# Optimization experiments

Hardware: AMD Instinct MI355X
Metric: run time of the kernel (lower is better)

The kernel has to match this reference:

```python
import jax, jax.numpy as jnp
import numpy as np

N_NODES, N_EDGES, N_GRAPHS, H = 20000, 160000, 256, 128
EPS = 1e-5


def setup_inputs() -> dict:
    key = jax.random.key(0)
    it = iter(jax.random.split(key, 64))

    def nk():
        return next(it)

    def lin(fan_in, wshape, bshape):
        s = 1.0 / np.sqrt(fan_in)
        W = jax.random.uniform(nk(), wshape, jnp.float32, -s, s)
        b = jax.random.uniform(nk(), bshape, jnp.float32, -s, s)
        return W, b

    def bn_params(shape):
        g = 1.0 + 0.1 * jax.random.normal(nk(), shape, jnp.float32)
        b = 0.1 * jax.random.normal(nk(), shape, jnp.float32)
        m = 0.1 * jax.random.normal(nk(), shape, jnp.float32)
        v = jax.random.uniform(nk(), shape, jnp.float32, 0.5, 1.5)
        return g, b, m, v

    inp = {}
    inp["x"] = jax.random.normal(nk(), (N_NODES, 10), jnp.float32)
    inp["edge_attr"] = jax.random.normal(nk(), (N_EDGES, 3), jnp.float32)
    inp["edge_index"] = jax.random.randint(nk(), (2, N_EDGES), 0, N_NODES)
    inp["batch"] = jnp.sort(jax.random.randint(nk(), (N_NODES,), 0, N_GRAPHS))
    inp["W_node"], inp["b_node"] = lin(10, (10, H), (H,))
    inp["W_edge"], inp["b_edge"] = lin(3, (3, H), (H,))
    # 10 stacked CGConv layers: lin_f / lin_s each map [2H + H] -> H
    inp["Wf"], inp["bf"] = lin(3 * H, (10, 3 * H, H), (10, H))
    inp["Ws"], inp["bs"] = lin(3 * H, (10, 3 * H, H), (10, H))
    inp["bn_g"], inp["bn_b"], inp["bn_m"], inp["bn_v"] = bn_params((10, H))
    inp["W1"], inp["b1"] = lin(3 * H, (3 * H, 2 * H), (2 * H,))
    inp["bn1_g"], inp["bn1_b"], inp["bn1_m"], inp["bn1_v"] = bn_params((2 * H,))
    inp["W2"], inp["b2"] = lin(2 * H, (2 * H, H), (H,))
    inp["bn2_g"], inp["bn2_b"], inp["bn2_m"], inp["bn2_v"] = bn_params((H,))
    inp["W3"], inp["b3"] = lin(H, (H, H // 2), (H // 2,))
    inp["Wv"], inp["bv"] = lin(H // 2, (H // 2, 1), (1,))
    inp["W_en"], inp["b_en"] = lin(H // 2, (H // 2, 1), (1,))
    inp["Wd"], inp["bd"] = lin(H // 2, (H // 2, 1), (1,))
    inp["Wh"], inp["bh"] = lin(H // 2, (H // 2, 1), (1,))
    return inp


def reference(x, edge_attr, edge_index, batch, W_node, b_node, W_edge, b_edge,
              Wf, bf, Ws, bs, bn_g, bn_b, bn_m, bn_v,
              W1, b1, bn1_g, bn1_b, bn1_m, bn1_v,
              W2, b2, bn2_g, bn2_b, bn2_m, bn2_v,
              W3, b3, Wv, bv, W_en, b_en, Wd, bd, Wh, bh):
    h = jax.nn.relu(x @ W_node + b_node)             # [N, H]
    e = jax.nn.relu(edge_attr @ W_edge + b_edge)     # [E, H]
    src, dst = edge_index[0], edge_index[1]          # PyG: messages src -> dst
    n = h.shape[0]
    for i in range(10):  # fixed layer count, structurally distinct weights
        h_in = h
        z = jnp.concatenate([h[dst], h[src], e], axis=1)          # [E, 3H] = [x_i, x_j, e_ij]
        msg = jax.nn.sigmoid(z @ Wf[i] + bf[i]) * jax.nn.softplus(z @ Ws[i] + bs[i])
        h = h_in + jax.ops.segment_sum(msg, dst, num_segments=n)  # CGConv residual + add-aggr
        h = (h - bn_m[i]) * (bn_g[i] / jnp.sqrt(bn_v[i] + EPS)) + bn_b[i]  # BN (eval)
        h = jax.nn.relu(h)  # dropout is identity in eval
        if i % 2 == 1:
            h = h + h_in
    # global mean / max / add pooling over graphs
    s = jax.ops.segment_sum(h, batch, num_segments=N_GRAPHS)                     # [G, H]
    cnt = jax.ops.segment_sum(jnp.ones((n, 1), h.dtype), batch, num_segments=N_GRAPHS)
    mean = s / jnp.maximum(cnt, 1.0)
    mx = jax.ops.segment_max(h, batch, num_segments=N_GRAPHS)
    g = jnp.concatenate([mean, mx, s], axis=1)                                   # [G, 3H]
    g = jax.nn.relu((g @ W1 + b1 - bn1_m) * (bn1_g / jnp.sqrt(bn1_v + EPS)) + bn1_b)
    g = jax.nn.relu((g @ W2 + b2 - bn2_m) * (bn2_g / jnp.sqrt(bn2_v + EPS)) + bn2_b)
    g = jax.nn.relu(g @ W3 + b3)
    return (g @ Wv + bv, g @ W_en + b_en, g @ Wd + bd, g @ Wh + bh)
```

## Files before the change

kernel.cpp:

```cpp
#include <hip/hip_runtime.h>
#include <hip/hip_bf16.h>
#include <math.h>

#define NN 20000
#define NE 160000
#define NG 256
#define EPSV 1e-5f
#define NQB 2500

typedef short bf16x8 __attribute__((ext_vector_type(8)));
typedef unsigned short u16x8 __attribute__((ext_vector_type(8)));
typedef float f32x4 __attribute__((ext_vector_type(4)));

__device__ __forceinline__ unsigned short f2bf(float f){
  unsigned int u = __float_as_uint(f);
  unsigned int r = (u + 0x7fffu + ((u>>16)&1u)) >> 16;
  return (unsigned short)r;
}
__device__ __forceinline__ float bf2f(unsigned short h){
  return __uint_as_float(((unsigned int)h) << 16);
}
__device__ __forceinline__ float fastmsg(float f, float sv){
  float sg = __builtin_amdgcn_rcpf(1.0f + __expf(-f));
  float sp = fmaxf(sv, 0.0f) + __logf(1.0f + __expf(-fabsf(sv)));
  return sg * sp;
}

__global__ __launch_bounds__(256) void k_hist(const int* __restrict__ ei, int* __restrict__ deg){
  int e = blockIdx.x*256 + threadIdx.x;
  if (e < NE) atomicAdd(&deg[ei[NE+e]], 1);
}
__global__ __launch_bounds__(1024) void k_scan(const int* __restrict__ deg,
                                               int* __restrict__ start, int* __restrict__ cur){
  __shared__ int part[1024];
  int t = threadIdx.x;
  int base = t*20;
  int s = 0;
  for (int j=0;j<20;j++){ int i = base+j; if (i<NN) s += deg[i]; }
  part[t] = s; __syncthreads();
  for (int off=1; off<1024; off<<=1){
    int v = (t >= off) ? part[t-off] : 0;
    __syncthreads();
    part[t] += v;
    __syncthreads();
  }
  int run = (t>0) ? part[t-1] : 0;
  for (int j=0;j<20;j++){
    int i = base+j;
    if (i<NN){ start[i] = run; cur[i] = run; run += deg[i]; }
  }
}
__global__ __launch_bounds__(256) void k_scatter(
    const int* __restrict__ ei, const float* __restrict__ eattr,
    int* __restrict__ cur, int* __restrict__ ei_s, int* __restrict__ ei_d,
    float* __restrict__ ea_s){
  int e = blockIdx.x*256 + threadIdx.x;
  if (e >= NE) return;
  int d = ei[NE+e];
  int p = atomicAdd(&cur[d], 1);
  ei_s[p] = ei[e]; ei_d[p] = d;
  ea_s[p*3+0] = eattr[e*3+0];
  ea_s[p*3+1] = eattr[e*3+1];
  ea_s[p*3+2] = eattr[e*3+2];
}

__global__ __launch_bounds__(256) void k_pack_w(
    const float* __restrict__ Wf, const float* __restrict__ Ws,
    unsigned short* __restrict__ Wpk_hi, unsigned short* __restrict__ Wpk_md,
    unsigned short* __restrict__ Wpk_lo)
{
  int idx = blockIdx.x*256 + threadIdx.x;
  if (idx >= 122880) return;
  int l = idx & 63, ks = (idx>>6)&3, nt = (idx>>8)&7;
  int m = idx >> 11;
  int blk = m % 3, gL = m / 3;
  int g = gL & 1, L = gL >> 1;
  const float* src = (g ? Ws : Wf) + (size_t)L*384*128;
  size_t off = (size_t)m*16384 + (nt*4+ks)*512 + l*8;
  int col = nt*16 + (l&15), k0 = ks*32 + (l>>4)*8;
  #pragma unroll
  for (int j=0;j<8;j++){
    float w = src[(size_t)(blk*128 + k0 + j)*128 + col];
    unsigned short hi = f2bf(w);
    float r1 = w - bf2f(hi);
    unsigned short md = f2bf(r1);
    float r2 = r1 - bf2f(md);
    Wpk_hi[off+j] = hi;
    Wpk_md[off+j] = md;
    Wpk_lo[off+j] = f2bf(r2);
  }
}

__global__ __launch_bounds__(256) void k_embed_node(
    const float* __restrict__ x, const float* __restrict__ W, const float* __restrict__ b,
    float* __restrict__ h, float* __restrict__ hacc)
{
  int i = blockIdx.x*256 + threadIdx.x;
  if (i >= NN*128) return;
  int n = i >> 7, c = i & 127;
  float acc = b[c];
  const float* xr = x + n*10;
  #pragma unroll
  for (int k=0;k<10;k++) acc = fmaf(xr[k], W[k*128+c], acc);
  acc = fmaxf(acc, 0.0f);
  h[i] = acc; hacc[i] = acc;
}

__global__ __launch_bounds__(512,1) void k_nodeproj_mfma(
    const float* __restrict__ h,
    const unsigned short* __restrict__ Wpk_hi, const unsigned short* __restrict__ Wpk_md,
    const unsigned short* __restrict__ Wpk_lo,
    const float* __restrict__ bfv, const float* __restrict__ bsv,
    float* __restrict__ Pd, float* __restrict__ Ps)
{
  __shared__ unsigned short wsm[49152];
  int bid = blockIdx.x;
  int m_idx = bid / 157, nblk = bid - m_idx*157;
  int mm = (m_idx==0)?0:(m_idx==1)?1:(m_idx==2)?3:4;
  int t = threadIdx.x;
  {
    const unsigned short* s0 = Wpk_hi + (size_t)mm*16384;
    const unsigned short* s1 = Wpk_md + (size_t)mm*16384;
    const unsigned short* s2 = Wpk_lo + (size_t)mm*16384;
    #pragma unroll
    for (int ii=0; ii<4; ii++){
      int o = (t + ii*512)*8;
      *(u16x8*)(wsm + o)         = *(const u16x8*)(s0 + o);
      *(u16x8*)(wsm + 16384 + o) = *(const u16x8*)(s1 + o);
      *(u16x8*)(wsm + 32768 + o) = *(const u16x8*)(s2 + o);
    }
  }
  __syncthreads();
  int l = t & 63, w = t >> 6;
  int nb = nblk*128 + w*16;
  if (nb + 16 > NN) return;
  const float* hb = h + (size_t)(nb + (l&15))*128 + (l>>4)*8;
  bf16x8 ah[4], am[4], al[4];
  #pragma unroll
  for (int ks=0;ks<4;ks++){
    #pragma unroll
    for (int j=0;j<8;j++){
      float v = hb[ks*32 + j];
      unsigned short x0 = f2bf(v);
      float r1 = v - bf2f(x0);
      unsigned short x1 = f2bf(r1);
      float r2 = r1 - bf2f(x1);
      ah[ks][j] = (short)x0; am[ks][j] = (short)x1; al[ks][j] = (short)f2bf(r2);
    }
  }
  float* OUT = (m_idx & 1) ? Ps : Pd;
  int sel = (m_idx >= 2) ? 1 : 0;
  const float* bias = (m_idx==0) ? bfv : (m_idx==2) ? bsv : nullptr;
  int col0 = l & 15, rg = (l>>4)*4;
  #pragma unroll
  for (int nt=0; nt<8; nt++){
    f32x4 c = {0.f,0.f,0.f,0.f};
    #pragma unroll
    for (int ks=0;ks<4;ks++){
      int fo = (nt*4+ks)*512 + l*8;
      bf16x8 bh = *(const bf16x8*)(wsm + fo);
      bf16x8 bm = *(const bf16x8*)(wsm + 16384 + fo);
      bf16x8 bl = *(const bf16x8*)(wsm + 32768 + fo);
      c = __builtin_amdgcn_mfma_f32_16x16x32_bf16(al[ks], bh, c, 0,0,0);
      c = __builtin_amdgcn_mfma_f32_16x16x32_bf16(am[ks], bm, c, 0,0,0);
      c = __builtin_amdgcn_mfma_f32_16x16x32_bf16(ah[ks], bl, c, 0,0,0);
      c = __builtin_amdgcn_mfma_f32_16x16x32_bf16(am[ks], bh, c, 0,0,0);
      c = __builtin_amdgcn_mfma_f32_16x16x32_bf16(ah[ks], bm, c, 0,0,0);
      c = __builtin_amdgcn_mfma_f32_16x16x32_bf16(ah[ks], bh, c, 0,0,0);
    }
    float bb = bias ? bias[nt*16+col0] : 0.0f;
    #pragma unroll
    for (int r=0;r<4;r++)
      OUT[(size_t)(nb+rg+r)*256 + (nt*16+col0)*2 + sel] = c[r] + bb;
  }
}

__global__ __launch_bounds__(256,4) void k_edge_mfma(
    const float* __restrict__ ea_s, const float* __restrict__ W_edge,
    const float* __restrict__ b_edge,
    const unsigned short* __restrict__ Wpk_hi,
    const unsigned short* __restrict__ Wpk_md,
    const int* __restrict__ ei_s, const int* __restrict__ ei_d,
    const float* __restrict__ Pd, const float* __restrict__ Ps,
    float* __restrict__ hacc)
{
  __shared__ float wlds[512];
  __shared__ unsigned short bfr[16384];
  int bid = blockIdx.x;
  int q = bid / NQB, eg = bid - q*NQB;
  int t = threadIdx.x;
  for (int i=t;i<512;i+=256) wlds[i] = (i<384)? W_edge[i] : b_edge[i-384];
  #pragma unroll
  for (int ii=0; ii<8; ii++){
    int idx = t + ii*256;
    int f = idx >> 6;
    int off = (idx & 63) * 8;
    int g = f >> 4, term = (f>>3)&1, ntl = (f>>2)&1, ks = f&3;
    const unsigned short* src = (term ? Wpk_md : Wpk_hi)
        + (size_t)(g?5:2)*16384 + (size_t)((((q*2+ntl)*4+ks)*512) + off);
    *(u16x8*)(bfr + f*512 + off) = *(const u16x8*)src;
  }
  __syncthreads();
  int l = t & 63, w = t >> 6;
  int e0 = eg*64;
  int row_edge = e0 + w*16 + (l&15);
  float a0 = ea_s[row_edge*3+0], a1 = ea_s[row_edge*3+1], a2 = ea_s[row_edge*3+2];
  int cbase = (l>>4)*8;
  bf16x8 ah[4], al[4];
  #pragma unroll
  for (int ks=0;ks<4;ks++){
    #pragma unroll
    for (int j=0;j<8;j++){
      int c = cbase + ks*32 + j;
      float v = fmaf(a0, wlds[c], fmaf(a1, wlds[128+c], fmaf(a2, wlds[256+c], wlds[384+c])));
      v = fmaxf(v, 0.0f);
      unsigned short hi = f2bf(v);
      ah[ks][j] = (short)hi;
      al[ks][j] = (short)f2bf(v - bf2f(hi));
    }
  }
  f32x4 accf[2], accs[2];
  #pragma unroll
  for (int ntl=0; ntl<2; ntl++){
    f32x4 cf = {0.f,0.f,0.f,0.f}, cs = {0.f,0.f,0.f,0.f};
    #pragma unroll
    for (int ks=0; ks<4; ks++){
      bf16x8 bh = *(const bf16x8*)(bfr + ((0<<4)|(0<<3)|(ntl<<2)|ks)*512 + l*8);
      bf16x8 bm = *(const bf16x8*)(bfr + ((0<<4)|(1<<3)|(ntl<<2)|ks)*512 + l*8);
      cf = __builtin_amdgcn_mfma_f32_16x16x32_bf16(ah[ks], bh, cf, 0,0,0);
      cf = __builtin_amdgcn_mfma_f32_16x16x32_bf16(ah[ks], bm, cf, 0,0,0);
      cf = __builtin_amdgcn_mfma_f32_16x16x32_bf16(al[ks], bh, cf, 0,0,0);
      bf16x8 sh = *(const bf16x8*)(bfr + ((1<<4)|(0<<3)|(ntl<<2)|ks)*512 + l*8);
      bf16x8 sm = *(const bf16x8*)(bfr + ((1<<4)|(1<<3)|(ntl<<2)|ks)*512 + l*8);
      cs = __builtin_amdgcn_mfma_f32_16x16x32_bf16(ah[ks], sh, cs, 0,0,0);
      cs = __builtin_amdgcn_mfma_f32_16x16x32_bf16(ah[ks], sm, cs, 0,0,0);
      cs = __builtin_amdgcn_mfma_f32_16x16x32_bf16(al[ks], sh, cs, 0,0,0);
    }
    accf[ntl] = cf; accs[ntl] = cs;
  }
  int eb = e0 + w*16, col0 = l & 15, rg = (l>>4)*4;
  int cA = (q*2+0)*16 + col0;
  int cB = (q*2+1)*16 + col0;
  int prev_d = -1;
  float m0 = 0.f, m1 = 0.f;
  float2 pd0, pd1;
  #pragma unroll
  for (int r=0;r<4;r++){
    int p = eb + rg + r;
    int s = ei_s[p], d = ei_d[p];
    if (d != prev_d){
      if (prev_d >= 0){
        atomicAdd(hacc + (size_t)prev_d*128 + cA, m0);
        atomicAdd(hacc + (size_t)prev_d*128 + cB, m1);
      }
      prev_d = d;
      pd0 = *(const float2*)(Pd + (size_t)d*256 + cA*2);
      pd1 = *(const float2*)(Pd + (size_t)d*256 + cB*2);
      m0 = 0.f; m1 = 0.f;
    }
    float2 ps0 = *(const float2*)(Ps + (size_t)s*256 + cA*2);
    float2 ps1 = *(const float2*)(Ps + (size_t)s*256 + cB*2);
    m0 += fastmsg(accf[0][r] + pd0.x + ps0.x, accs[0][r] + pd0.y + ps0.y);
    m1 += fastmsg(accf[1][r] + pd1.x + ps1.x, accs[1][r] + pd1.y + ps1.y);
  }
  atomicAdd(hacc + (size_t)prev_d*128 + cA, m0);
  atomicAdd(hacc + (size_t)prev_d*128 + cB, m1);
}

__global__ __launch_bounds__(256) void k_bn(
    const float* __restrict__ hacc, const float* __restrict__ hin,
    const float* __restrict__ gam, const float* __restrict__ bet,
    const float* __restrict__ mu, const float* __restrict__ var,
    float* __restrict__ hout, float* __restrict__ haccout, int addres)
{
  int i = blockIdx.x*256 + threadIdx.x;
  if (i >= NN*128) return;
  int c = i & 127;
  float scale = gam[c]*rsqrtf(var[c]+EPSV);
  float tv = (hacc[i]-mu[c])*scale + bet[c];
  tv = fmaxf(tv, 0.0f);
  if (addres) tv += hin[i];
  hout[i] = tv; haccout[i] = tv;
}

__global__ __launch_bounds__(256) void k_pool(
    const float* __restrict__ h, const int* __restrict__ batch,
    float* __restrict__ psum, float* __restrict__ pmax, float* __restrict__ pcnt)
{
  int i = blockIdx.x*256 + threadIdx.x;
  if (i >= NN*128) return;
  int n = i >> 7, c = i & 127;
  int b = batch[n];
  float v = h[i];
  atomicAdd(&psum[b*128+c], v);
  atomicMax((unsigned int*)&pmax[b*128+c], __float_as_uint(v));
  if (c == 0) atomicAdd(&pcnt[b], 1.0f);
}

__global__ __launch_bounds__(256) void k_mlp1(
    const float* __restrict__ psum, const float* __restrict__ pmax, const float* __restrict__ pcnt,
    const float* __restrict__ W1, const float* __restrict__ b1,
    const float* __restrict__ g1g, const float* __restrict__ g1b,
    const float* __restrict__ g1m, const float* __restrict__ g1v,
    float* __restrict__ out)
{
  int i = blockIdx.x*256 + threadIdx.x;
  int g = i >> 8, c = i & 255;
  float inv = 1.0f / fmaxf(pcnt[g], 1.0f);
  float acc = b1[c];
  for (int k=0;k<128;k++) acc = fmaf(psum[g*128+k]*inv, W1[k*256+c], acc);
  for (int k=0;k<128;k++) acc = fmaf(pmax[g*128+k],     W1[(128+k)*256+c], acc);
  for (int k=0;k<128;k++) acc = fmaf(psum[g*128+k],     W1[(256+k)*256+c], acc);
  float scale = g1g[c]*rsqrtf(g1v[c]+EPSV);
  acc = (acc - g1m[c])*scale + g1b[c];
  out[i] = fmaxf(acc, 0.0f);
}

__global__ __launch_bounds__(256) void k_mlp2(
    const float* __restrict__ g1, const float* __restrict__ W2, const float* __restrict__ b2,
    const float* __restrict__ g2g, const float* __restrict__ g2b,
    const float* __restrict__ g2m, const float* __restrict__ g2v,
    float* __restrict__ out)
{
  int i = blockIdx.x*256 + threadIdx.x;
  int g = i >> 7, c = i & 127;
  float acc = b2[c];
  for (int k=0;k<256;k++) acc = fmaf(g1[g*256+k], W2[k*128+c], acc);
  float scale = g2g[c]*rsqrtf(g2v[c]+EPSV);
  acc = (acc - g2m[c])*scale + g2b[c];
  out[i] = fmaxf(acc, 0.0f);
}

__global__ __launch_bounds__(256) void k_mlp3(
    const float* __restrict__ g2, const float* __restrict__ W3, const float* __restrict__ b3,
    float* __restrict__ out)
{
  int i = blockIdx.x*256 + threadIdx.x;
  int g = i >> 6, c = i & 63;
  float acc = b3[c];
  for (int k=0;k<128;k++) acc = fmaf(g2[g*128+k], W3[k*64+c], acc);
  out[i] = fmaxf(acc, 0.0f);
}

__global__ __launch_bounds__(256) void k_heads(
    const float* __restrict__ g3,
    const float* __restrict__ Wv, const float* __restrict__ bv,
    const float* __restrict__ We, const float* __restrict__ be,
    const float* __restrict__ Wd, const float* __restrict__ bd,
    const float* __restrict__ Wh, const float* __restrict__ bh,
    float* __restrict__ out)
{
  int g = blockIdx.x*256 + threadIdx.x;
  if (g >= NG) return;
  float a0=bv[0], a1=be[0], a2=bd[0], a3=bh[0];
  for (int k=0;k<64;k++){
    float xv = g3[g*64+k];
    a0 = fmaf(xv, Wv[k], a0);
    a1 = fmaf(xv, We[k], a1);
    a2 = fmaf(xv, Wd[k], a2);
    a3 = fmaf(xv, Wh[k], a3);
  }
  out[g] = a0; out[NG+g] = a1; out[2*NG+g] = a2; out[3*NG+g] = a3;
}

extern "C" void kernel_launch(void* const* d_in, const int* in_sizes, int n_in,
                              void* d_out, int out_size, void* d_ws, size_t ws_size,
                              hipStream_t stream)
{
  const float* x         = (const float*)d_in[0];
  const float* edge_attr = (const float*)d_in[1];
  const int*   ei        = (const int*)d_in[2];
  const int*   batch     = (const int*)d_in[3];
  const float* W_node    = (const float*)d_in[4];
  const float* b_node    = (const float*)d_in[5];
  const float* W_edge    = (const float*)d_in[6];
  const float* b_edge    = (const float*)d_in[7];
  const float* Wf        = (const float*)d_in[8];
  const float* bf        = (const float*)d_in[9];
  const float* Ws        = (const float*)d_in[10];
  const float* bs        = (const float*)d_in[11];
  const float* bn_g      = (const float*)d_in[12];
  const float* bn_b      = (const float*)d_in[13];
  const float* bn_m      = (const float*)d_in[14];
  const float* bn_v      = (const float*)d_in[15];
  const float* W1        = (const float*)d_in[16];
  const float* b1        = (const float*)d_in[17];
  const float* bn1_g     = (const float*)d_in[18];
  const float* bn1_b     = (const float*)d_in[19];
  const float* bn1_m     = (const float*)d_in[20];
  const float* bn1_v     = (const float*)d_in[21];
  const float* W2        = (const float*)d_in[22];
  const float* b2        = (const float*)d_in[23];
  const float* bn2_g     = (const float*)d_in[24];
  const float* bn2_b     = (const float*)d_in[25];
  const float* bn2_m     = (const float*)d_in[26];
  const float* bn2_v     = (const float*)d_in[27];
  const float* W3        = (const float*)d_in[28];
  const float* b3        = (const float*)d_in[29];
  const float* Wv        = (const float*)d_in[30];
  const float* bv        = (const float*)d_in[31];
  const float* W_en      = (const float*)d_in[32];
  const float* b_en      = (const float*)d_in[33];
  const float* Wd        = (const float*)d_in[34];
  const float* bd        = (const float*)d_in[35];
  const float* Wh        = (const float*)d_in[36];
  const float* bh        = (const float*)d_in[37];

  float* wsf  = (float*)d_ws;
  float* h    = wsf;
  float* hacc = wsf + 2560000;
  float* Pd   = wsf + 5120000;
  float* Ps   = wsf + 10240000;
  unsigned short* Wpk_hi = (unsigned short*)(wsf + 15360000);
  unsigned short* Wpk_md = (unsigned short*)(wsf + 15851520);
  unsigned short* Wpk_lo = (unsigned short*)(wsf + 16343040);
  float* psum = wsf + 16834560;
  float* pmax = psum + 32768;
  float* pcnt = pmax + 32768;
  float* g1   = pcnt + 256;
  float* g2   = g1 + 65536;
  float* g3   = g2 + 32768;
  int*   deg  = (int*)(wsf + 16982272);
  int*   start= deg + 20000;
  int*   cur  = start + 20000;
  int*   ei_s = cur + 20000;
  int*   ei_d = ei_s + 160000;
  float* ea_s = (float*)(ei_d + 160000);

  hipMemsetAsync(deg, 0, 20000*sizeof(int), stream);
  k_hist<<<(NE+255)/256, 256, 0, stream>>>(ei, deg);
  k_scan<<<1, 1024, 0, stream>>>(deg, start, cur);
  k_scatter<<<(NE+255)/256, 256, 0, stream>>>(ei, edge_attr, cur, ei_s, ei_d, ea_s);

  k_pack_w<<<480, 256, 0, stream>>>(Wf, Ws, Wpk_hi, Wpk_md, Wpk_lo);
  k_embed_node<<<(NN*128+255)/256, 256, 0, stream>>>(x, W_node, b_node, h, hacc);
  hipMemsetAsync(psum, 0, (size_t)(32768+32768+256)*sizeof(float), stream);

  for (int i=0;i<10;i++){
    const unsigned short* WH = Wpk_hi + (size_t)i*6*16384;
    const unsigned short* WM = Wpk_md + (size_t)i*6*16384;
    const unsigned short* WL = Wpk_lo + (size_t)i*6*16384;
    k_nodeproj_mfma<<<628, 512, 0, stream>>>(h, WH, WM, WL,
        bf + i*128, bs + i*128, Pd, Ps);
    k_edge_mfma<<<4*NQB, 256, 0, stream>>>(ea_s, W_edge, b_edge,
        WH, WM, ei_s, ei_d, Pd, Ps, hacc);
    k_bn<<<(NN*128+255)/256, 256, 0, stream>>>(hacc, h,
        bn_g + i*128, bn_b + i*128, bn_m + i*128, bn_v + i*128, h, hacc, i&1);
  }

  k_pool<<<(NN*128+255)/256, 256, 0, stream>>>(h, batch, psum, pmax, pcnt);
  k_mlp1<<<(NG*256)/256, 256, 0, stream>>>(psum, pmax, pcnt, W1, b1, bn1_g, bn1_b, bn1_m, bn1_v, g1);
  k_mlp2<<<(NG*128)/256, 256, 0, stream>>>(g1, W2, b2, bn2_g, bn2_b, bn2_m, bn2_v, g2);
  k_mlp3<<<(NG*64)/256, 256, 0, stream>>>(g2, W3, b3, g3);
  k_heads<<<1, 256, 0, stream>>>(g3, Wv, bv, W_en, b_en, Wd, bd, Wh, bh, (float*)d_out);
}
```

Measured before the change: 1.424 ms.

## Cut nodeproj LDS to raise occupancy, pack edge indices, fuse final BN with pooling

The node projection kernel now keeps only the hi and mid weight planes in LDS and reads the lo plane straight from global memory. This shrinks shared memory so two blocks can run per CU, at the cost of extra global or cache traffic per MFMA step. The bf16 hi and mid splits now truncate instead of round, which saves instructions while keeping the three-term split exact enough. Source and destination indices are packed into one int2 array so each edge needs a single load, and the last layer's BN is fused with global pooling, removing one elementwise pass and one launch.

Result: faster. 1.302 ms (-8.6%).

```diff
diff --git a/kernel.cpp b/kernel.cpp
--- a/kernel.cpp
+++ b/kernel.cpp
@@ -52,13 +52,12 @@
 }
 __global__ __launch_bounds__(256) void k_scatter(
     const int* __restrict__ ei, const float* __restrict__ eattr,
-    int* __restrict__ cur, int* __restrict__ ei_s, int* __restrict__ ei_d,
-    float* __restrict__ ea_s){
+    int* __restrict__ cur, int2* __restrict__ esd, float* __restrict__ ea_s){
   int e = blockIdx.x*256 + threadIdx.x;
   if (e >= NE) return;
   int d = ei[NE+e];
   int p = atomicAdd(&cur[d], 1);
-  ei_s[p] = ei[e]; ei_d[p] = d;
+  esd[p] = make_int2(ei[e], d);
   ea_s[p*3+0] = eattr[e*3+0];
   ea_s[p*3+1] = eattr[e*3+1];
   ea_s[p*3+2] = eattr[e*3+2];
@@ -106,14 +105,14 @@
   h[i] = acc; hacc[i] = acc;
 }
 
-__global__ __launch_bounds__(512,1) void k_nodeproj_mfma(
+__global__ __launch_bounds__(512,2) void k_nodeproj_mfma(
     const float* __restrict__ h,
     const unsigned short* __restrict__ Wpk_hi, const unsigned short* __restrict__ Wpk_md,
     const unsigned short* __restrict__ Wpk_lo,
     const float* __restrict__ bfv, const float* __restrict__ bsv,
     float* __restrict__ Pd, float* __restrict__ Ps)
 {
-  __shared__ unsigned short wsm[49152];
+  __shared__ unsigned short wsm[32768];
   int bid = blockIdx.x;
   int m_idx = bid / 157, nblk = bid - m_idx*157;
   int mm = (m_idx==0)?0:(m_idx==1)?1:(m_idx==2)?3:4;
@@ -121,13 +120,11 @@
   {
     const unsigned short* s0 = Wpk_hi + (size_t)mm*16384;
     const unsigned short* s1 = Wpk_md + (size_t)mm*16384;
-    const unsigned short* s2 = Wpk_lo + (size_t)mm*16384;
     #pragma unroll
     for (int ii=0; ii<4; ii++){
       int o = (t + ii*512)*8;
       *(u16x8*)(wsm + o)         = *(const u16x8*)(s0 + o);
       *(u16x8*)(wsm + 16384 + o) = *(const u16x8*)(s1 + o);
-      *(u16x8*)(wsm + 32768 + o) = *(const u16x8*)(s2 + o);
     }
   }
   __syncthreads();
@@ -141,13 +138,14 @@
     #pragma unroll
     for (int j=0;j<8;j++){
       float v = hb[ks*32 + j];
-      unsigned short x0 = f2bf(v);
+      unsigned short x0 = (unsigned short)(__float_as_uint(v) >> 16);
       float r1 = v - bf2f(x0);
-      unsigned short x1 = f2bf(r1);
+      unsigned short x1 = (unsigned short)(__float_as_uint(r1) >> 16);
       float r2 = r1 - bf2f(x1);
       ah[ks][j] = (short)x0; am[ks][j] = (short)x1; al[ks][j] = (short)f2bf(r2);
     }
   }
+  const unsigned short* wl = Wpk_lo + (size_t)mm*16384 + l*8;
   float* OUT = (m_idx & 1) ? Ps : Pd;
   int sel = (m_idx >= 2) ? 1 : 0;
   const float* bias = (m_idx==0) ? bfv : (m_idx==2) ? bsv : nullptr;
@@ -160,7 +158,7 @@
       int fo = (nt*4+ks)*512 + l*8;
       bf16x8 bh = *(const bf16x8*)(wsm + fo);
       bf16x8 bm = *(const bf16x8*)(wsm + 16384 + fo);
-      bf16x8 bl = *(const bf16x8*)(wsm + 32768 + fo);
+      bf16x8 bl = *(const bf16x8*)(wl + (nt*4+ks)*512);
       c = __builtin_amdgcn_mfma_f32_16x16x32_bf16(al[ks], bh, c, 0,0,0);
       c = __builtin_amdgcn_mfma_f32_16x16x32_bf16(am[ks], bm, c, 0,0,0);
       c = __builtin_amdgcn_mfma_f32_16x16x32_bf16(ah[ks], bl, c, 0,0,0);
@@ -180,7 +178,7 @@
     const float* __restrict__ b_edge,
     const unsigned short* __restrict__ Wpk_hi,
     const unsigned short* __restrict__ Wpk_md,
-    const int* __restrict__ ei_s, const int* __restrict__ ei_d,
+    const int2* __restrict__ esd,
     const float* __restrict__ Pd, const float* __restrict__ Ps,
     float* __restrict__ hacc)
 {
@@ -214,7 +212,7 @@
       int c = cbase + ks*32 + j;
       float v = fmaf(a0, wlds[c], fmaf(a1, wlds[128+c], fmaf(a2, wlds[256+c], wlds[384+c])));
       v = fmaxf(v, 0.0f);
-      unsigned short hi = f2bf(v);
+      unsigned short hi = (unsigned short)(__float_as_uint(v) >> 16);
       ah[ks][j] = (short)hi;
       al[ks][j] = (short)f2bf(v - bf2f(hi));
     }
@@ -247,7 +245,8 @@
   #pragma unroll
   for (int r=0;r<4;r++){
     int p = eb + rg + r;
-    int s = ei_s[p], d = ei_d[p];
+    int2 sd = esd[p];
+    int s = sd.x, d = sd.y;
     if (d != prev_d){
       if (prev_d >= 0){
         atomicAdd(hacc + (size_t)prev_d*128 + cA, m0);
@@ -283,17 +282,24 @@
   hout[i] = tv; haccout[i] = tv;
 }
 
-__global__ __launch_bounds__(256) void k_pool(
-    const float* __restrict__ h, const int* __restrict__ batch,
-    float* __restrict__ psum, float* __restrict__ pmax, float* __restrict__ pcnt)
+__global__ __launch_bounds__(256) void k_bn_pool(
+    const float* __restrict__ hacc, const float* __restrict__ hin,
+    const float* __restrict__ gam, const float* __restrict__ bet,
+    const float* __restrict__ mu, const float* __restrict__ var,
+    const int* __restrict__ batch,
+    float* __restrict__ psum, float* __restrict__ pmax, float* __restrict__ pcnt,
+    int addres)
 {
   int i = blockIdx.x*256 + threadIdx.x;
   if (i >= NN*128) return;
   int n = i >> 7, c = i & 127;
+  float scale = gam[c]*rsqrtf(var[c]+EPSV);
+  float tv = (hacc[i]-mu[c])*scale + bet[c];
+  tv = fmaxf(tv, 0.0f);
+  if (addres) tv += hin[i];
   int b = batch[n];
-  float v = h[i];
-  atomicAdd(&psum[b*128+c], v);
-  atomicMax((unsigned int*)&pmax[b*128+c], __float_as_uint(v));
+  atomicAdd(&psum[b*128+c], tv);
+  atomicMax((unsigned int*)&pmax[b*128+c], __float_as_uint(tv));
   if (c == 0) atomicAdd(&pcnt[b], 1.0f);
 }
 
@@ -423,14 +429,13 @@
   int*   deg  = (int*)(wsf + 16982272);
   int*   start= deg + 20000;
   int*   cur  = start + 20000;
-  int*   ei_s = cur + 20000;
-  int*   ei_d = ei_s + 160000;
-  float* ea_s = (float*)(ei_d + 160000);
+  int2*  esd  = (int2*)(cur + 20000);
+  float* ea_s = (float*)(cur + 20000 + 320000);
 
   hipMemsetAsync(deg, 0, 20000*sizeof(int), stream);
   k_hist<<<(NE+255)/256, 256, 0, stream>>>(ei, deg);
   k_scan<<<1, 1024, 0, stream>>>(deg, start, cur);
-  k_scatter<<<(NE+255)/256, 256, 0, stream>>>(ei, edge_attr, cur, ei_s, ei_d, ea_s);
+  k_scatter<<<(NE+255)/256, 256, 0, stream>>>(ei, edge_attr, cur, esd, ea_s);
 
   k_pack_w<<<480, 256, 0, stream>>>(Wf, Ws, Wpk_hi, Wpk_md, Wpk_lo);
   k_embed_node<<<(NN*128+255)/256, 256, 0, stream>>>(x, W_node, b_node, h, hacc);
@@ -443,12 +448,16 @@
     k_nodeproj_mfma<<<628, 512, 0, stream>>>(h, WH, WM, WL,
         bf + i*128, bs + i*128, Pd, Ps);
     k_edge_mfma<<<4*NQB, 256, 0, stream>>>(ea_s, W_edge, b_edge,
-        WH, WM, ei_s, ei_d, Pd, Ps, hacc);
-    k_bn<<<(NN*128+255)/256, 256, 0, stream>>>(hacc, h,
-        bn_g + i*128, bn_b + i*128, bn_m + i*128, bn_v + i*128, h, hacc, i&1);
-  }
-
-  k_pool<<<(NN*128+255)/256, 256, 0, stream>>>(h, batch, psum, pmax, pcnt);
+        WH, WM, esd, Pd, Ps, hacc);
+    if (i < 9)
+      k_bn<<<(NN*128+255)/256, 256, 0, stream>>>(hacc, h,
+          bn_g + i*128, bn_b + i*128, bn_m + i*128, bn_v + i*128, h, hacc, i&1);
+    else
+      k_bn_pool<<<(NN*128+255)/256, 256, 0, stream>>>(hacc, h,
+          bn_g + i*128, bn_b + i*128, bn_m + i*128, bn_v + i*128,
+          batch, psum, pmax, pcnt, i&1);
+  }
+
   k_mlp1<<<(NG*256)/256, 256, 0, stream>>>(psum, pmax, pcnt, W1, b1, bn1_g, bn1_b, bn1_m, bn1_v, g1);
   k_mlp2<<<(NG*128)/256, 256, 0, stream>>>(g1, W2, b2, bn2_g, bn2_b, bn2_m, bn2_v, g2);
   k_mlp3<<<(NG*64)/256, 256, 0, stream>>>(g2, W3, b3, g3);
```
